# Kernel optimization log

Measured on AMD Instinct MI355X. Metric: run time of the kernel, lower is better.

## Reference

```python
import jax, jax.numpy as jnp
import numpy as np


def setup_inputs() -> dict:
    key = jax.random.key(0)
    # [3, B, H, N, d] stacked q, k, v
    qkv = jax.random.normal(key, (3, 4, 8, 4096, 32), dtype=jnp.float32)
    return {"qkv": qkv}


def reference(qkv):
    q, k, v = qkv[0], qkv[1], qkv[2]  # each [B, H, N, d]
    # kv_mod = box(k,k)^T @ v  -> [B,H,d,d,d] (avoids materializing [B,H,N,d^2])
    kv2 = jnp.einsum('bhnd,bhne,bhnf->bhdef', k, k, v)
    # k^T @ v -> [B,H,d,d]
    kv1 = jnp.einsum('bhnd,bhnf->bhdf', k, v)
    v_sum = jnp.sum(v, axis=-2, keepdims=True)  # [B,H,1,d]
    k_sum = jnp.sum(k, axis=-2)                 # [B,H,d]
    # y = 0.5 * box(q,q) @ kv_mod + q @ (k^T v) + sum(v)
    y = (0.5 * jnp.einsum('bhnd,bhne,bhdef->bhnf', q, q, kv2)
         + jnp.einsum('bhnd,bhdf->bhnf', q, kv1)
         + v_sum)
    # y_norm: box(q,q) . box(k_sum,k_sum) == (q . k_sum)^2
    qk = jnp.einsum('bhnd,bhd->bhn', q, k_sum)  # [B,H,N]
    y_norm = 0.5 * qk * qk + qk + 1.0
    return y / y_norm[..., None]
```

## Files before the change

kernel.cpp:

```cpp
#include <hip/hip_runtime.h>

#define NTOK 4096
#define DIM 32
#define NBH 32

#define BHF1 18496
#define SLOT1 591872
#define SUMOFF1 18432
#define KCH1 16
#define TSF 260
#define TSH 264

#define KCH 18
#define PK_U32 (NBH * KCH * 1024)
#define PK_HALF (PK_U32 / 2)
#define P2TOK 128

#define NPAIR2 528
#define NROWS 560
#define BHF (NROWS * 32 + 64)
#define SLOT (NBH * BHF)
#define TILE 64
#define LSTR 36
#define P1T 320

typedef __attribute__((ext_vector_type(8))) short bf16x8;
typedef __attribute__((ext_vector_type(8))) _Float16 f16x8;
typedef __attribute__((ext_vector_type(4))) float f32x4;
typedef __attribute__((ext_vector_type(4))) unsigned u32x4;

__device__ __forceinline__ int tri_start(int d) { return (d * (65 - d)) >> 1; }

__device__ __forceinline__ int tri_decode_d(int p) {
    int d = (int)((65.0f - sqrtf((float)(4225 - 8 * p))) * 0.5f);
    if (d < 0) d = 0;
    if (d > 31) d = 31;
    while (d < 31 && tri_start(d + 1) <= p) ++d;
    while (d > 0 && tri_start(d) > p) --d;
    return d;
}

__device__ __forceinline__ void row_operands(int row, int& ia, int& ib) {
    if (row < NPAIR2) {
        const int d = tri_decode_d(row);
        ia = d; ib = d + (row - tri_start(d));
    } else if (row < NROWS) {
        ia = row - NPAIR2; ib = 32;
    } else {
        ia = 34; ib = 34;
    }
}

__device__ __forceinline__ unsigned short f2bf(float x) {
    unsigned u = __builtin_bit_cast(unsigned, x);
    return (unsigned short)((u + 0x7FFFu + ((u >> 16) & 1u)) >> 16);
}
__device__ __forceinline__ float bf2f(unsigned short u) {
    return __builtin_bit_cast(float, (unsigned)u << 16);
}

__device__ __forceinline__ void split8(const float* p, f16x8& hi, f16x8& lo) {
#pragma unroll
    for (int j = 0; j < 8; ++j) {
        const _Float16 h = (_Float16)p[j];
        hi[j] = h;
        lo[j] = (_Float16)(p[j] - (float)h);
    }
}

#define MF(A, B, C) __builtin_amdgcn_mfma_f32_16x16x32_f16((A), (B), (C), 0, 0, 0)

__global__ __launch_bounds__(256) void phase1m_kernel(const float* __restrict__ qkv,
                                                      float* __restrict__ ws) {
    const int chunk = blockIdx.x;
    const int bh = blockIdx.y;
    const int t = threadIdx.x;
    const int w = t >> 6, l = t & 63, g = l >> 4, c16 = l & 15;

    __shared__ float skT[32 * TSF];
    __shared__ _Float16 svhiT[32 * TSH];
    __shared__ _Float16 svloT[32 * TSH];

    {
        const float4* kg4 = (const float4*)(qkv + (size_t)(NBH + bh) * (NTOK * DIM) + (size_t)chunk * 256 * DIM);
        const float4* vg4 = (const float4*)(qkv + (size_t)(2 * NBH + bh) * (NTOK * DIM) + (size_t)chunk * 256 * DIM);
#pragma unroll
        for (int j = 0; j < 8; ++j) {
            const int i = t + 256 * j;
            const int tok = i >> 3, dbase = (i & 7) << 2;
            const float4 kf = kg4[i];
            const float4 vf = vg4[i];
            const float ke[4] = {kf.x, kf.y, kf.z, kf.w};
            const float ve[4] = {vf.x, vf.y, vf.z, vf.w};
#pragma unroll
            for (int c = 0; c < 4; ++c) {
                skT[(dbase + c) * TSF + tok] = ke[c];
                const _Float16 h = (_Float16)ve[c];
                svhiT[(dbase + c) * TSH + tok] = h;
                svloT[(dbase + c) * TSH + tok] = (_Float16)(ve[c] - (float)h);
            }
        }
    }
    __syncthreads();

    f32x4 acc[4][2][2];
    f32x4 accS[2][2];
#pragma unroll
    for (int i = 0; i < 4; ++i)
#pragma unroll
        for (int m = 0; m < 2; ++m)
#pragma unroll
            for (int fh = 0; fh < 2; ++fh) acc[i][m][fh] = (f32x4){0.f, 0.f, 0.f, 0.f};
#pragma unroll
    for (int m = 0; m < 2; ++m)
#pragma unroll
        for (int fh = 0; fh < 2; ++fh) accS[m][fh] = (f32x4){0.f, 0.f, 0.f, 0.f};

    const f16x8 ones = {(_Float16)1.f, (_Float16)1.f, (_Float16)1.f, (_Float16)1.f,
                        (_Float16)1.f, (_Float16)1.f, (_Float16)1.f, (_Float16)1.f};

#pragma unroll 1
    for (int n0 = 0; n0 < 256; n0 += 32) {
        const int sl = n0 + 8 * g;
        float a0[8], a1[8];
        *(float4*)&a0[0] = *(const float4*)(skT + c16 * TSF + sl);
        *(float4*)&a0[4] = *(const float4*)(skT + c16 * TSF + sl + 4);
        *(float4*)&a1[0] = *(const float4*)(skT + (16 + c16) * TSF + sl);
        *(float4*)&a1[4] = *(const float4*)(skT + (16 + c16) * TSF + sl + 4);
        const f16x8 Bh0 = *(const f16x8*)(svhiT + c16 * TSH + sl);
        const f16x8 Bh1 = *(const f16x8*)(svhiT + (16 + c16) * TSH + sl);
        const f16x8 Bl0 = *(const f16x8*)(svloT + c16 * TSH + sl);
        const f16x8 Bl1 = *(const f16x8*)(svloT + (16 + c16) * TSH + sl);

#pragma unroll
        for (int i = 0; i < 4; ++i) {
            const int o = w + 4 * i;
            const int r0 = ((c16 + o) & 31) * TSF;
            const int r1 = ((16 + c16 + o) & 31) * TSF;
            float e0[8], e1[8], p0[8], p1[8];
            *(float4*)&e0[0] = *(const float4*)(skT + r0 + sl);
            *(float4*)&e0[4] = *(const float4*)(skT + r0 + sl + 4);
            *(float4*)&e1[0] = *(const float4*)(skT + r1 + sl);
            *(float4*)&e1[4] = *(const float4*)(skT + r1 + sl + 4);
#pragma unroll
            for (int j = 0; j < 8; ++j) { p0[j] = a0[j] * e0[j]; p1[j] = a1[j] * e1[j]; }
            f16x8 A0h, A0l, A1h, A1l;
            split8(p0, A0h, A0l);
            split8(p1, A1h, A1l);
            acc[i][0][0] = MF(A0h, Bh0, acc[i][0][0]);
            acc[i][0][0] = MF(A0l, Bh0, acc[i][0][0]);
            acc[i][0][0] = MF(A0h, Bl0, acc[i][0][0]);
            acc[i][0][1] = MF(A0h, Bh1, acc[i][0][1]);
            acc[i][0][1] = MF(A0l, Bh1, acc[i][0][1]);
            acc[i][0][1] = MF(A0h, Bl1, acc[i][0][1]);
            acc[i][1][0] = MF(A1h, Bh0, acc[i][1][0]);
            acc[i][1][0] = MF(A1l, Bh0, acc[i][1][0]);
            acc[i][1][0] = MF(A1h, Bl0, acc[i][1][0]);
            acc[i][1][1] = MF(A1h, Bh1, acc[i][1][1]);
            acc[i][1][1] = MF(A1l, Bh1, acc[i][1][1]);
            acc[i][1][1] = MF(A1h, Bl1, acc[i][1][1]);
        }

        if (w == 0) {
            float p[8];
#pragma unroll
            for (int j = 0; j < 8; ++j) p[j] = a0[j] * a1[j];
            f16x8 Ah, Al;
            split8(p, Ah, Al);
            accS[0][0] = MF(Ah, Bh0, accS[0][0]);
            accS[0][0] = MF(Al, Bh0, accS[0][0]);
            accS[0][0] = MF(Ah, Bl0, accS[0][0]);
            accS[0][1] = MF(Ah, Bh1, accS[0][1]);
            accS[0][1] = MF(Al, Bh1, accS[0][1]);
            accS[0][1] = MF(Ah, Bl1, accS[0][1]);
        } else if (w == 1) {
            f16x8 K0h, K0l, K1h, K1l;
            split8(a0, K0h, K0l);
            split8(a1, K1h, K1l);
            accS[0][0] = MF(K0h, Bh0, accS[0][0]);
            accS[0][0] = MF(K0l, Bh0, accS[0][0]);
            accS[0][0] = MF(K0h, Bl0, accS[0][0]);
            accS[0][1] = MF(K0h, Bh1, accS[0][1]);
            accS[0][1] = MF(K0l, Bh1, accS[0][1]);
            accS[0][1] = MF(K0h, Bl1, accS[0][1]);
            accS[1][0] = MF(K1h, Bh0, accS[1][0]);
            accS[1][0] = MF(K1l, Bh0, accS[1][0]);
            accS[1][0] = MF(K1h, Bl0, accS[1][0]);
            accS[1][1] = MF(K1h, Bh1, accS[1][1]);
            accS[1][1] = MF(K1l, Bh1, accS[1][1]);
            accS[1][1] = MF(K1h, Bl1, accS[1][1]);
        } else if (w == 2) {
            f16x8 K0h, K0l, K1h, K1l;
            split8(a0, K0h, K0l);
            split8(a1, K1h, K1l);
            accS[0][0] = MF(ones, K0h, accS[0][0]);
            accS[0][0] = MF(ones, K0l, accS[0][0]);
            accS[1][0] = MF(ones, K1h, accS[1][0]);
            accS[1][0] = MF(ones, K1l, accS[1][0]);
        } else {
            accS[0][0] = MF(ones, Bh0, accS[0][0]);
            accS[0][0] = MF(ones, Bl0, accS[0][0]);
            accS[0][1] = MF(ones, Bh1, accS[0][1]);
            accS[0][1] = MF(ones, Bl1, accS[0][1]);
        }
    }

    float* pb = ws + (size_t)SLOT1 * (1 + chunk) + (size_t)bh * BHF1;
#pragma unroll
    for (int i = 0; i < 4; ++i) {
        const int o = w + 4 * i;
#pragma unroll
        for (int m = 0; m < 2; ++m)
#pragma unroll
            for (int fh = 0; fh < 2; ++fh)
#pragma unroll
                for (int r = 0; r < 4; ++r) {
                    const int R = o * 32 + 16 * m + 4 * g + r;
                    pb[(size_t)R * 32 + fh * 16 + c16] = acc[i][m][fh][r];
                }
    }
    if (w == 0) {
#pragma unroll
        for (int fh = 0; fh < 2; ++fh)
#pragma unroll
            for (int r = 0; r < 4; ++r) {
                const int R = 512 + 4 * g + r;
                pb[(size_t)R * 32 + fh * 16 + c16] = accS[0][fh][r];
                pb[(size_t)(R + 16) * 32 + fh * 16 + c16] = accS[0][fh][r];
            }
    } else if (w == 1) {
#pragma unroll
        for (int m = 0; m < 2; ++m)
#pragma unroll
            for (int fh = 0; fh < 2; ++fh)
#pragma unroll
                for (int r = 0; r < 4; ++r) {
                    const int R = 544 + 16 * m + 4 * g + r;
                    pb[(size_t)R * 32 + fh * 16 + c16] = accS[m][fh][r];
                }
    } else if (w == 2) {
        if (g == 0) {
            pb[SUMOFF1 + c16] = accS[0][0][0];
            pb[SUMOFF1 + 16 + c16] = accS[1][0][0];
        }
    } else {
        if (g == 0) {
            pb[SUMOFF1 + 32 + c16] = accS[0][0][0];
            pb[SUMOFF1 + 48 + c16] = accS[0][1][0];
        }
    }
}

__global__ __launch_bounds__(256) void reduceprep_kernel(const float* __restrict__ ws,
                                                         float* __restrict__ wsw,
                                                         unsigned* __restrict__ bpk) {
    const int tid = blockIdx.x * 256 + threadIdx.x;
    if (tid < PK_HALF) {
        const int r = tid & 3;
        const int l = (tid >> 2) & 63;
        const int fh = (tid >> 8) & 1;
        const int kcbh = tid >> 9;
        const int kc = kcbh % KCH;
        const int bh = kcbh / KCH;
        const int f = fh * 16 + (l & 15);
        const int k0 = kc * 32 + ((l >> 4) << 3) + 2 * r;
        const float scale = (kc == 0 || kc == 16) ? 0.5f : 1.0f;
        float va = 0.f, vb = 0.f;
        const float* src = ws + (size_t)bh * BHF1 + (size_t)k0 * 32 + f;
#pragma unroll
        for (int c = 1; c <= KCH1; ++c) {
            va += src[(size_t)SLOT1 * c];
            vb += src[(size_t)SLOT1 * c + 32];
        }
        va *= scale; vb *= scale;
        const _Float16 ha = (_Float16)va, hb = (_Float16)vb;
        const _Float16 la = (_Float16)(va - (float)ha), lb = (_Float16)(vb - (float)hb);
        const int widx = ((bh * KCH + kc) * 2 + fh) * 512 + l * 4 + r;
        bpk[widx] = (unsigned)__builtin_bit_cast(unsigned short, ha) |
                    ((unsigned)__builtin_bit_cast(unsigned short, hb) << 16);
        bpk[widx + 256] = (unsigned)__builtin_bit_cast(unsigned short, la) |
                          ((unsigned)__builtin_bit_cast(unsigned short, lb) << 16);
    } else {
        const int tid2 = tid - PK_HALF;
        if (tid2 < NBH * 64) {
            const int bh = tid2 >> 6;
            const int j = tid2 & 63;
            float s = 0.f;
            const float* src = ws + (size_t)bh * BHF1 + SUMOFF1 + j;
#pragma unroll
            for (int c = 1; c <= KCH1; ++c) s += src[(size_t)SLOT1 * c];
            wsw[(size_t)bh * BHF1 + SUMOFF1 + j] = s;
        }
    }
}

#define EMIT_PHI() do { \
    unsigned hh[16]; \
    _Pragma("unroll") \
    for (int kp = 0; kp < 16; ++kp) { \
        const _Float16 h0 = (_Float16)phi[2 * kp]; \
        const _Float16 h1 = (_Float16)phi[2 * kp + 1]; \
        hh[kp] = (unsigned)__builtin_bit_cast(unsigned short, h0) | \
                 ((unsigned)__builtin_bit_cast(unsigned short, h1) << 16); \
    } \
    _Pragma("unroll") \
    for (int c4 = 0; c4 < 4; ++c4) { \
        u32x4 vh = {hh[4*c4], hh[4*c4+1], hh[4*c4+2], hh[4*c4+3]}; \
        *(u32x4*)&sph[t * 20 + c4 * 4] = vh; \
    } \
} while (0)

#define MFMA_CHUNK(KC) do { \
    const unsigned* bc = bbase + (size_t)(KC) * 1024; \
    const f16x8 Bh0 = __builtin_bit_cast(f16x8, *(const u32x4*)(bc + 0   + l * 4)); \
    const f16x8 Bl0 = __builtin_bit_cast(f16x8, *(const u32x4*)(bc + 256 + l * 4)); \
    const f16x8 Bh1 = __builtin_bit_cast(f16x8, *(const u32x4*)(bc + 512 + l * 4)); \
    const f16x8 Bl1 = __builtin_bit_cast(f16x8, *(const u32x4*)(bc + 768 + l * 4)); \
    _Pragma("unroll") \
    for (int T = 0; T < 4; ++T) { \
        const int ro = (wbase + T * 16 + arow) * 20 + acol; \
        const f16x8 Ah = __builtin_bit_cast(f16x8, *(const u32x4*)&sph[ro]); \
        acc[T][0] = MF(Ah, Bh0, acc[T][0]); \
        acc[T][0] = MF(Ah, Bl0, acc[T][0]); \
        acc[T][1] = MF(Ah, Bh1, acc[T][1]); \
        acc[T][1] = MF(Ah, Bl1, acc[T][1]); \
    } \
} while (0)

__global__ __launch_bounds__(P2TOK) void phase2m_kernel(const float* __restrict__ qkv,
                                                        const float* __restrict__ ws,
                                                        const unsigned* __restrict__ bpk,
                                                        float* __restrict__ out) {
    const int bh = blockIdx.y;
    const int tok0 = blockIdx.x * P2TOK;
    const int t = threadIdx.x;
    const int l = t & 63;
    const int wbase = (t >> 6) << 6;
    const int arow = l & 15;
    const int acol = (l >> 4) << 2;

    __shared__ unsigned sph[P2TOK * 20];
    __shared__ float sinv[P2TOK];

    float q[32];
    {
        const float4* q4 = (const float4*)(qkv + ((size_t)bh * NTOK + tok0 + t) * DIM);
#pragma unroll
        for (int i = 0; i < 8; ++i) {
            const float4 v = q4[i];
            q[4 * i + 0] = v.x; q[4 * i + 1] = v.y; q[4 * i + 2] = v.z; q[4 * i + 3] = v.w;
        }
    }
    {
        const float* ks = ws + (size_t)bh * BHF1 + SUMOFF1;
        float qk = 0.f;
#pragma unroll
        for (int d = 0; d < 32; ++d) qk += q[d] * ks[d];
        sinv[t] = 1.0f / (0.5f * qk * qk + qk + 1.0f);
    }

    f32x4 acc[4][2];
#pragma unroll
    for (int T = 0; T < 4; ++T)
#pragma unroll
        for (int fh = 0; fh < 2; ++fh) acc[T][fh] = (f32x4){0.f, 0.f, 0.f, 0.f};

    const unsigned* bbase = bpk + (size_t)bh * (KCH * 1024);

    {
        float qr[32];
#pragma unroll
        for (int j2 = 0; j2 < 32; ++j2) qr[j2] = q[j2];
#pragma unroll 1
        for (int kc = 0; kc < 17; ++kc) {
            float phi[32];
#pragma unroll
            for (int j2 = 0; j2 < 32; ++j2) phi[j2] = q[j2] * qr[j2];
            EMIT_PHI();
            MFMA_CHUNK(kc);
            const float tmp = qr[0];
#pragma unroll
            for (int j2 = 0; j2 < 31; ++j2) qr[j2] = qr[j2 + 1];
            qr[31] = tmp;
        }
    }
    {
        float phi[32];
#pragma unroll
        for (int j2 = 0; j2 < 32; ++j2) phi[j2] = q[j2];
        EMIT_PHI();
        MFMA_CHUNK(17);
    }

    const float* vs = ws + (size_t)bh * BHF1 + SUMOFF1 + 32;
    const float vs0 = vs[l & 15];
    const float vs1 = vs[16 + (l & 15)];
#pragma unroll
    for (int T = 0; T < 4; ++T) {
#pragma unroll
        for (int r = 0; r < 4; ++r) {
            const int row = wbase + T * 16 + ((l >> 4) << 2) + r;
            const float iv = sinv[row];
            float* op = out + ((size_t)bh * NTOK + tok0 + row) * DIM + (l & 15);
            op[0]  = (acc[T][0][r] + vs0) * iv;
            op[16] = (acc[T][1][r] + vs1) * iv;
        }
    }
}

__global__ __launch_bounds__(P1T) void phase1_kernel(const float* __restrict__ qkv,
                                                     float* __restrict__ ws, int direct) {
    const int chunk = blockIdx.x;
    const int bh = blockIdx.y;
    const int CHt = NTOK / gridDim.x;
    const int t = threadIdx.x;
    const float* kptr = qkv + (size_t)(NBH + bh) * (NTOK * DIM);
    const float* vptr = qkv + (size_t)(2 * NBH + bh) * (NTOK * DIM);
    float* base = ws + (direct ? (size_t)0 : (size_t)SLOT * (1 + chunk)) + (size_t)bh * BHF;

    __shared__ __align__(16) float sk[TILE][LSTR];
    __shared__ __align__(16) float sv[TILE][LSTR];

    int ia0, ib0, ia1, ib1;
    row_operands(t, ia0, ib0);
    row_operands(t + P1T, ia1, ib1);
    const float* a0 = &sk[0][ia0];
    const float* b0 = &sk[0][ib0];
    const float* a1 = &sk[0][ia1];
    const float* b1 = &sk[0][ib1];
    const float* sums = (t >= 288) ? &sv[0][t - 288] : ((t >= 256) ? &sk[0][t - 256] : &sk[0][0]);

    float acc0[32], acc1[32];
#pragma unroll
    for (int f = 0; f < 32; ++f) { acc0[f] = 0.f; acc1[f] = 0.f; }
    float accs = 0.f;

    if (t < 64) sk[t][32] = 1.0f;
    else if (t < 128) sk[t - 64][34] = 0.0f;

    const int n0 = chunk * CHt;
    for (int nt = 0; nt < CHt; nt += TILE) {
        __syncthreads();
        if (t < 256) {
            const float4* kg4 = (const float4*)(kptr + (size_t)(n0 + nt) * DIM);
            const float4* vg4 = (const float4*)(vptr + (size_t)(n0 + nt) * DIM);
            const int i0 = t, i1 = t + 256;
            *(float4*)&sk[i0 >> 3][(i0 & 7) << 2] = kg4[i0];
            *(float4*)&sk[i1 >> 3][(i1 & 7) << 2] = kg4[i1];
            *(float4*)&sv[i0 >> 3][(i0 & 7) << 2] = vg4[i0];
            *(float4*)&sv[i1 >> 3][(i1 & 7) << 2] = vg4[i1];
        }
        __syncthreads();
#pragma unroll 2
        for (int nn = 0; nn < TILE; ++nn) {
            const float s0 = a0[nn * LSTR] * b0[nn * LSTR];
            const float s1 = a1[nn * LSTR] * b1[nn * LSTR];
            const float* vrow = vptr + (size_t)(n0 + nt + nn) * DIM;
            float4 w[8];
#pragma unroll
            for (int j = 0; j < 8; ++j) w[j] = ((const float4*)vrow)[j];
#pragma unroll
            for (int j = 0; j < 8; ++j) {
                acc0[4 * j + 0] += s0 * w[j].x; acc0[4 * j + 1] += s0 * w[j].y;
                acc0[4 * j + 2] += s0 * w[j].z; acc0[4 * j + 3] += s0 * w[j].w;
                acc1[4 * j + 0] += s1 * w[j].x; acc1[4 * j + 1] += s1 * w[j].y;
                acc1[4 * j + 2] += s1 * w[j].z; acc1[4 * j + 3] += s1 * w[j].w;
            }
            if (t >= 256) accs += sums[nn * LSTR];
        }
    }

    {
        float* dst = base + (size_t)t * 32;
#pragma unroll
        for (int j = 0; j < 8; ++j) {
            float4 v; v.x = acc0[4 * j]; v.y = acc0[4 * j + 1];
            v.z = acc0[4 * j + 2]; v.w = acc0[4 * j + 3];
            ((float4*)dst)[j] = v;
        }
    }
    if (t < 240) {
        float* dst = base + (size_t)(t + P1T) * 32;
#pragma unroll
        for (int j = 0; j < 8; ++j) {
            float4 v; v.x = acc1[4 * j]; v.y = acc1[4 * j + 1];
            v.z = acc1[4 * j + 2]; v.w = acc1[4 * j + 3];
            ((float4*)dst)[j] = v;
        }
    }
    if (t >= 256) base[NROWS * 32 + (t - 256)] = accs;
}

__global__ __launch_bounds__(256) void phase2_kernel(const float* __restrict__ qkv,
                                                     const float* __restrict__ ws,
                                                     float* __restrict__ out) {
    const int bh = blockIdx.y;
    const int f0 = blockIdx.z << 4;
    const int t = threadIdx.x;
    const int tok0 = blockIdx.x * 256;
    const float* qptr = qkv + (size_t)bh * (NTOK * DIM) + (size_t)tok0 * DIM;
    const float* base = ws + (size_t)bh * BHF;
    const float* ksum = base + NROWS * 32;
    const float* vsum = ksum + 32;

    __shared__ float qT[32][256];
    {
        const float4* q4 = (const float4*)qptr + (size_t)t * 8;
#pragma unroll
        for (int i = 0; i < 8; ++i) {
            const float4 v = q4[i];
            qT[4 * i + 0][t] = v.x; qT[4 * i + 1][t] = v.y;
            qT[4 * i + 2][t] = v.z; qT[4 * i + 3][t] = v.w;
        }
    }
    __syncthreads();

    float y[16];
#pragma unroll
    for (int j = 0; j < 4; ++j) {
        const float4 v = *(const float4*)(vsum + f0 + 4 * j);
        y[4 * j + 0] = v.x; y[4 * j + 1] = v.y; y[4 * j + 2] = v.z; y[4 * j + 3] = v.w;
    }
    float qk = 0.f;
    const float* rowp = base + f0;
#pragma unroll 1
    for (int d = 0; d < 32; ++d) {
        const float qd = qT[d][t];
        qk += qd * ksum[d];
        {
            const float s = 0.5f * qd * qd;
            const float4* r = (const float4*)rowp;
#pragma unroll
            for (int j = 0; j < 4; ++j) {
                const float4 w = r[j];
                y[4 * j + 0] += s * w.x; y[4 * j + 1] += s * w.y;
                y[4 * j + 2] += s * w.z; y[4 * j + 3] += s * w.w;
            }
            rowp += 32;
        }
#pragma unroll 4
        for (int e = d + 1; e < 32; ++e) {
            const float s = qd * qT[e][t];
            const float4* r = (const float4*)rowp;
#pragma unroll
            for (int j = 0; j < 4; ++j) {
                const float4 w = r[j];
                y[4 * j + 0] += s * w.x; y[4 * j + 1] += s * w.y;
                y[4 * j + 2] += s * w.z; y[4 * j + 3] += s * w.w;
            }
            rowp += 32;
        }
    }
#pragma unroll 4
    for (int d = 0; d < 32; ++d) {
        const float qd = qT[d][t];
        const float4* r = (const float4*)rowp;
#pragma unroll
        for (int j = 0; j < 4; ++j) {
            const float4 w = r[j];
            y[4 * j + 0] += qd * w.x; y[4 * j + 1] += qd * w.y;
            y[4 * j + 2] += qd * w.z; y[4 * j + 3] += qd * w.w;
        }
        rowp += 32;
    }
    const float inv = 1.0f / (0.5f * qk * qk + qk + 1.0f);
    float4* o4 = (float4*)(out + (size_t)bh * (NTOK * DIM) + (size_t)(tok0 + t) * DIM + f0);
#pragma unroll
    for (int j = 0; j < 4; ++j) {
        float4 v;
        v.x = y[4 * j + 0] * inv; v.y = y[4 * j + 1] * inv;
        v.z = y[4 * j + 2] * inv; v.w = y[4 * j + 3] * inv;
        o4[j] = v;
    }
}

extern "C" void kernel_launch(void* const* d_in, const int* in_sizes, int n_in,
                              void* d_out, int out_size, void* d_ws, size_t ws_size,
                              hipStream_t stream) {
    const float* qkv = (const float*)d_in[0];
    float* out = (float*)d_out;
    float* ws = (float*)d_ws;

    const size_t need = ((size_t)(1 + KCH1) * SLOT1 + PK_U32) * 4;
    if (ws_size >= need) {
        unsigned* bpk = (unsigned*)(ws + (size_t)(1 + KCH1) * SLOT1);
        phase1m_kernel<<<dim3(KCH1, NBH), dim3(256), 0, stream>>>(qkv, ws);
        reduceprep_kernel<<<dim3((PK_HALF + NBH * 64) / 256), dim3(256), 0, stream>>>(ws, ws, bpk);
        phase2m_kernel<<<dim3(NTOK / P2TOK, NBH), dim3(P2TOK), 0, stream>>>(qkv, ws, bpk, out);
    } else {
        phase1_kernel<<<dim3(1, NBH), dim3(P1T), 0, stream>>>(qkv, ws, 1);
        phase2_kernel<<<dim3(NTOK / 256, NBH, 2), dim3(256), 0, stream>>>(qkv, ws, out);
    }
}
```

Before: 62.84 us.

## Halve phase1 LDS staging, vectorize transposed stores, shrink phase2 blocks to one wave

Phase1 now stages K/V in two 128-token halves instead of one 256-token tile. Each thread loads four tokens for one feature quad and writes transposed rows with vector stores, which halves LDS use and replaces scalar transposed writes. Phase2 drops to 64 tokens per block (a single wave) and unrolls the feature-chunk loop by four, removing per-iteration register rotation. The changes add extra barriers in phase1 and launch twice as many smaller phase2 blocks.

```diff
diff --git a/kernel.cpp b/kernel.cpp
--- a/kernel.cpp
+++ b/kernel.cpp
@@ -8,13 +8,13 @@
 #define SLOT1 591872
 #define SUMOFF1 18432
 #define KCH1 16
-#define TSF 260
-#define TSH 264
+#define TSF2 132
+#define TSH2 136
 
 #define KCH 18
 #define PK_U32 (NBH * KCH * 1024)
 #define PK_HALF (PK_U32 / 2)
-#define P2TOK 128
+#define P2TOK 64
 
 #define NPAIR2 528
 #define NROWS 560
@@ -26,6 +26,7 @@
 
 typedef __attribute__((ext_vector_type(8))) short bf16x8;
 typedef __attribute__((ext_vector_type(8))) _Float16 f16x8;
+typedef __attribute__((ext_vector_type(4))) _Float16 f16x4;
 typedef __attribute__((ext_vector_type(4))) float f32x4;
 typedef __attribute__((ext_vector_type(4))) unsigned u32x4;
 
@@ -51,14 +52,6 @@
     }
 }
 
-__device__ __forceinline__ unsigned short f2bf(float x) {
-    unsigned u = __builtin_bit_cast(unsigned, x);
-    return (unsigned short)((u + 0x7FFFu + ((u >> 16) & 1u)) >> 16);
-}
-__device__ __forceinline__ float bf2f(unsigned short u) {
-    return __builtin_bit_cast(float, (unsigned)u << 16);
-}
-
 __device__ __forceinline__ void split8(const float* p, f16x8& hi, f16x8& lo) {
 #pragma unroll
     for (int j = 0; j < 8; ++j) {
@@ -77,31 +70,12 @@
     const int t = threadIdx.x;
     const int w = t >> 6, l = t & 63, g = l >> 4, c16 = l & 15;
 
-    __shared__ float skT[32 * TSF];
-    __shared__ _Float16 svhiT[32 * TSH];
-    __shared__ _Float16 svloT[32 * TSH];
-
-    {
-        const float4* kg4 = (const float4*)(qkv + (size_t)(NBH + bh) * (NTOK * DIM) + (size_t)chunk * 256 * DIM);
-        const float4* vg4 = (const float4*)(qkv + (size_t)(2 * NBH + bh) * (NTOK * DIM) + (size_t)chunk * 256 * DIM);
-#pragma unroll
-        for (int j = 0; j < 8; ++j) {
-            const int i = t + 256 * j;
-            const int tok = i >> 3, dbase = (i & 7) << 2;
-            const float4 kf = kg4[i];
-            const float4 vf = vg4[i];
-            const float ke[4] = {kf.x, kf.y, kf.z, kf.w};
-            const float ve[4] = {vf.x, vf.y, vf.z, vf.w};
-#pragma unroll
-            for (int c = 0; c < 4; ++c) {
-                skT[(dbase + c) * TSF + tok] = ke[c];
-                const _Float16 h = (_Float16)ve[c];
-                svhiT[(dbase + c) * TSH + tok] = h;
-                svloT[(dbase + c) * TSH + tok] = (_Float16)(ve[c] - (float)h);
-            }
-        }
-    }
-    __syncthreads();
+    __shared__ float skT[32 * TSF2];
+    __shared__ _Float16 svhiT[32 * TSH2];
+    __shared__ _Float16 svloT[32 * TSH2];
+
+    const float4* kg4 = (const float4*)(qkv + (size_t)(NBH + bh) * (NTOK * DIM)) + (size_t)chunk * 256 * 8;
+    const float4* vg4 = (const float4*)(qkv + (size_t)(2 * NBH + bh) * (NTOK * DIM)) + (size_t)chunk * 256 * 8;
 
     f32x4 acc[4][2][2];
     f32x4 accS[2][2];
@@ -119,89 +93,129 @@
     const f16x8 ones = {(_Float16)1.f, (_Float16)1.f, (_Float16)1.f, (_Float16)1.f,
                         (_Float16)1.f, (_Float16)1.f, (_Float16)1.f, (_Float16)1.f};
 
+    const int fq = t >> 5;
+    const int tq = t & 31;
+
 #pragma unroll 1
-    for (int n0 = 0; n0 < 256; n0 += 32) {
-        const int sl = n0 + 8 * g;
-        float a0[8], a1[8];
-        *(float4*)&a0[0] = *(const float4*)(skT + c16 * TSF + sl);
-        *(float4*)&a0[4] = *(const float4*)(skT + c16 * TSF + sl + 4);
-        *(float4*)&a1[0] = *(const float4*)(skT + (16 + c16) * TSF + sl);
-        *(float4*)&a1[4] = *(const float4*)(skT + (16 + c16) * TSF + sl + 4);
-        const f16x8 Bh0 = *(const f16x8*)(svhiT + c16 * TSH + sl);
-        const f16x8 Bh1 = *(const f16x8*)(svhiT + (16 + c16) * TSH + sl);
-        const f16x8 Bl0 = *(const f16x8*)(svloT + c16 * TSH + sl);
-        const f16x8 Bl1 = *(const f16x8*)(svloT + (16 + c16) * TSH + sl);
-
-#pragma unroll
-        for (int i = 0; i < 4; ++i) {
-            const int o = w + 4 * i;
-            const int r0 = ((c16 + o) & 31) * TSF;
-            const int r1 = ((16 + c16 + o) & 31) * TSF;
-            float e0[8], e1[8], p0[8], p1[8];
-            *(float4*)&e0[0] = *(const float4*)(skT + r0 + sl);
-            *(float4*)&e0[4] = *(const float4*)(skT + r0 + sl + 4);
-            *(float4*)&e1[0] = *(const float4*)(skT + r1 + sl);
-            *(float4*)&e1[4] = *(const float4*)(skT + r1 + sl + 4);
-#pragma unroll
-            for (int j = 0; j < 8; ++j) { p0[j] = a0[j] * e0[j]; p1[j] = a1[j] * e1[j]; }
-            f16x8 A0h, A0l, A1h, A1l;
-            split8(p0, A0h, A0l);
-            split8(p1, A1h, A1l);
-            acc[i][0][0] = MF(A0h, Bh0, acc[i][0][0]);
-            acc[i][0][0] = MF(A0l, Bh0, acc[i][0][0]);
-            acc[i][0][0] = MF(A0h, Bl0, acc[i][0][0]);
-            acc[i][0][1] = MF(A0h, Bh1, acc[i][0][1]);
-            acc[i][0][1] = MF(A0l, Bh1, acc[i][0][1]);
-            acc[i][0][1] = MF(A0h, Bl1, acc[i][0][1]);
-            acc[i][1][0] = MF(A1h, Bh0, acc[i][1][0]);
-            acc[i][1][0] = MF(A1l, Bh0, acc[i][1][0]);
-            acc[i][1][0] = MF(A1h, Bl0, acc[i][1][0]);
-            acc[i][1][1] = MF(A1h, Bh1, acc[i][1][1]);
-            acc[i][1][1] = MF(A1l, Bh1, acc[i][1][1]);
-            acc[i][1][1] = MF(A1h, Bl1, acc[i][1][1]);
-        }
-
-        if (w == 0) {
-            float p[8];
-#pragma unroll
-            for (int j = 0; j < 8; ++j) p[j] = a0[j] * a1[j];
-            f16x8 Ah, Al;
-            split8(p, Ah, Al);
-            accS[0][0] = MF(Ah, Bh0, accS[0][0]);
-            accS[0][0] = MF(Al, Bh0, accS[0][0]);
-            accS[0][0] = MF(Ah, Bl0, accS[0][0]);
-            accS[0][1] = MF(Ah, Bh1, accS[0][1]);
-            accS[0][1] = MF(Al, Bh1, accS[0][1]);
-            accS[0][1] = MF(Ah, Bl1, accS[0][1]);
-        } else if (w == 1) {
-            f16x8 K0h, K0l, K1h, K1l;
-            split8(a0, K0h, K0l);
-            split8(a1, K1h, K1l);
-            accS[0][0] = MF(K0h, Bh0, accS[0][0]);
-            accS[0][0] = MF(K0l, Bh0, accS[0][0]);
-            accS[0][0] = MF(K0h, Bl0, accS[0][0]);
-            accS[0][1] = MF(K0h, Bh1, accS[0][1]);
-            accS[0][1] = MF(K0l, Bh1, accS[0][1]);
-            accS[0][1] = MF(K0h, Bl1, accS[0][1]);
-            accS[1][0] = MF(K1h, Bh0, accS[1][0]);
-            accS[1][0] = MF(K1l, Bh0, accS[1][0]);
-            accS[1][0] = MF(K1h, Bl0, accS[1][0]);
-            accS[1][1] = MF(K1h, Bh1, accS[1][1]);
-            accS[1][1] = MF(K1l, Bh1, accS[1][1]);
-            accS[1][1] = MF(K1h, Bl1, accS[1][1]);
-        } else if (w == 2) {
-            f16x8 K0h, K0l, K1h, K1l;
-            split8(a0, K0h, K0l);
-            split8(a1, K1h, K1l);
-            accS[0][0] = MF(ones, K0h, accS[0][0]);
-            accS[0][0] = MF(ones, K0l, accS[0][0]);
-            accS[1][0] = MF(ones, K1h, accS[1][0]);
-            accS[1][0] = MF(ones, K1l, accS[1][0]);
-        } else {
-            accS[0][0] = MF(ones, Bh0, accS[0][0]);
-            accS[0][0] = MF(ones, Bl0, accS[0][0]);
-            accS[0][1] = MF(ones, Bh1, accS[0][1]);
-            accS[0][1] = MF(ones, Bl1, accS[0][1]);
+    for (int half = 0; half < 2; ++half) {
+        __syncthreads();
+        {
+            const int nb = half * 128;
+            float4 kf[4], vf[4];
+#pragma unroll
+            for (int c = 0; c < 4; ++c) {
+                kf[c] = kg4[(size_t)(nb + tq * 4 + c) * 8 + fq];
+                vf[c] = vg4[(size_t)(nb + tq * 4 + c) * 8 + fq];
+            }
+            const float kr[4][4] = {{kf[0].x, kf[1].x, kf[2].x, kf[3].x},
+                                    {kf[0].y, kf[1].y, kf[2].y, kf[3].y},
+                                    {kf[0].z, kf[1].z, kf[2].z, kf[3].z},
+                                    {kf[0].w, kf[1].w, kf[2].w, kf[3].w}};
+            const float vr[4][4] = {{vf[0].x, vf[1].x, vf[2].x, vf[3].x},
+                                    {vf[0].y, vf[1].y, vf[2].y, vf[3].y},
+                                    {vf[0].z, vf[1].z, vf[2].z, vf[3].z},
+                                    {vf[0].w, vf[1].w, vf[2].w, vf[3].w}};
+#pragma unroll
+            for (int r = 0; r < 4; ++r) {
+                *(float4*)(skT + (fq * 4 + r) * TSF2 + tq * 4) =
+                    (float4){kr[r][0], kr[r][1], kr[r][2], kr[r][3]};
+                f16x4 vh, vl;
+#pragma unroll
+                for (int c = 0; c < 4; ++c) {
+                    const _Float16 h = (_Float16)vr[r][c];
+                    vh[c] = h;
+                    vl[c] = (_Float16)(vr[r][c] - (float)h);
+                }
+                *(f16x4*)(svhiT + (fq * 4 + r) * TSH2 + tq * 4) = vh;
+                *(f16x4*)(svloT + (fq * 4 + r) * TSH2 + tq * 4) = vl;
+            }
+        }
+        __syncthreads();
+
+#pragma unroll 1
+        for (int it = 0; it < 4; ++it) {
+            const int sl = it * 32 + 8 * g;
+            float a0[8], a1[8];
+            *(float4*)&a0[0] = *(const float4*)(skT + c16 * TSF2 + sl);
+            *(float4*)&a0[4] = *(const float4*)(skT + c16 * TSF2 + sl + 4);
+            *(float4*)&a1[0] = *(const float4*)(skT + (16 + c16) * TSF2 + sl);
+            *(float4*)&a1[4] = *(const float4*)(skT + (16 + c16) * TSF2 + sl + 4);
+            const f16x8 Bh0 = *(const f16x8*)(svhiT + c16 * TSH2 + sl);
+            const f16x8 Bh1 = *(const f16x8*)(svhiT + (16 + c16) * TSH2 + sl);
+            const f16x8 Bl0 = *(const f16x8*)(svloT + c16 * TSH2 + sl);
+            const f16x8 Bl1 = *(const f16x8*)(svloT + (16 + c16) * TSH2 + sl);
+
+#pragma unroll
+            for (int i = 0; i < 4; ++i) {
+                const int o = w + 4 * i;
+                const int r0 = ((c16 + o) & 31) * TSF2;
+                const int r1 = ((16 + c16 + o) & 31) * TSF2;
+                float e0[8], e1[8], p0[8], p1[8];
+                *(float4*)&e0[0] = *(const float4*)(skT + r0 + sl);
+                *(float4*)&e0[4] = *(const float4*)(skT + r0 + sl + 4);
+                *(float4*)&e1[0] = *(const float4*)(skT + r1 + sl);
+                *(float4*)&e1[4] = *(const float4*)(skT + r1 + sl + 4);
+#pragma unroll
+                for (int j = 0; j < 8; ++j) { p0[j] = a0[j] * e0[j]; p1[j] = a1[j] * e1[j]; }
+                f16x8 A0h, A0l, A1h, A1l;
+                split8(p0, A0h, A0l);
+                split8(p1, A1h, A1l);
+                acc[i][0][0] = MF(A0h, Bh0, acc[i][0][0]);
+                acc[i][0][0] = MF(A0l, Bh0, acc[i][0][0]);
+                acc[i][0][0] = MF(A0h, Bl0, acc[i][0][0]);
+                acc[i][0][1] = MF(A0h, Bh1, acc[i][0][1]);
+                acc[i][0][1] = MF(A0l, Bh1, acc[i][0][1]);
+                acc[i][0][1] = MF(A0h, Bl1, acc[i][0][1]);
+                acc[i][1][0] = MF(A1h, Bh0, acc[i][1][0]);
+                acc[i][1][0] = MF(A1l, Bh0, acc[i][1][0]);
+                acc[i][1][0] = MF(A1h, Bl0, acc[i][1][0]);
+                acc[i][1][1] = MF(A1h, Bh1, acc[i][1][1]);
+                acc[i][1][1] = MF(A1l, Bh1, acc[i][1][1]);
+                acc[i][1][1] = MF(A1h, Bl1, acc[i][1][1]);
+            }
+
+            if (w == 0) {
+                float p[8];
+#pragma unroll
+                for (int j = 0; j < 8; ++j) p[j] = a0[j] * a1[j];
+                f16x8 Ah, Al;
+                split8(p, Ah, Al);
+                accS[0][0] = MF(Ah, Bh0, accS[0][0]);
+                accS[0][0] = MF(Al, Bh0, accS[0][0]);
+                accS[0][0] = MF(Ah, Bl0, accS[0][0]);
+                accS[0][1] = MF(Ah, Bh1, accS[0][1]);
+                accS[0][1] = MF(Al, Bh1, accS[0][1]);
+                accS[0][1] = MF(Ah, Bl1, accS[0][1]);
+            } else if (w == 1) {
+                f16x8 K0h, K0l, K1h, K1l;
+                split8(a0, K0h, K0l);
+                split8(a1, K1h, K1l);
+                accS[0][0] = MF(K0h, Bh0, accS[0][0]);
+                accS[0][0] = MF(K0l, Bh0, accS[0][0]);
+                accS[0][0] = MF(K0h, Bl0, accS[0][0]);
+                accS[0][1] = MF(K0h, Bh1, accS[0][1]);
+                accS[0][1] = MF(K0l, Bh1, accS[0][1]);
+                accS[0][1] = MF(K0h, Bl1, accS[0][1]);
+                accS[1][0] = MF(K1h, Bh0, accS[1][0]);
+                accS[1][0] = MF(K1l, Bh0, accS[1][0]);
+                accS[1][0] = MF(K1h, Bl0, accS[1][0]);
+                accS[1][1] = MF(K1h, Bh1, accS[1][1]);
+                accS[1][1] = MF(K1l, Bh1, accS[1][1]);
+                accS[1][1] = MF(K1h, Bl1, accS[1][1]);
+            } else if (w == 2) {
+                f16x8 K0h, K0l, K1h, K1l;
+                split8(a0, K0h, K0l);
+                split8(a1, K1h, K1l);
+                accS[0][0] = MF(ones, K0h, accS[0][0]);
+                accS[0][0] = MF(ones, K0l, accS[0][0]);
+                accS[1][0] = MF(ones, K1h, accS[1][0]);
+                accS[1][0] = MF(ones, K1l, accS[1][0]);
+            } else {
+                accS[0][0] = MF(ones, Bh0, accS[0][0]);
+                accS[0][0] = MF(ones, Bl0, accS[0][0]);
+                accS[0][1] = MF(ones, Bh1, accS[0][1]);
+                accS[0][1] = MF(ones, Bl1, accS[0][1]);
+            }
         }
     }
 
@@ -294,31 +308,31 @@
     }
 }
 
-#define EMIT_PHI() do { \
+#define EMIT_MFMA(PHIEXPR, KCEXPR) do { \
     unsigned hh[16]; \
     _Pragma("unroll") \
     for (int kp = 0; kp < 16; ++kp) { \
-        const _Float16 h0 = (_Float16)phi[2 * kp]; \
-        const _Float16 h1 = (_Float16)phi[2 * kp + 1]; \
+        const int j0 = 2 * kp, j1 = 2 * kp + 1; \
+        const float p0 = (PHIEXPR(j0)); \
+        const float p1 = (PHIEXPR(j1)); \
+        const _Float16 h0 = (_Float16)p0; \
+        const _Float16 h1 = (_Float16)p1; \
         hh[kp] = (unsigned)__builtin_bit_cast(unsigned short, h0) | \
                  ((unsigned)__builtin_bit_cast(unsigned short, h1) << 16); \
     } \
     _Pragma("unroll") \
     for (int c4 = 0; c4 < 4; ++c4) { \
-        u32x4 vh = {hh[4*c4], hh[4*c4+1], hh[4*c4+2], hh[4*c4+3]}; \
+        u32x4 vh = {hh[4 * c4], hh[4 * c4 + 1], hh[4 * c4 + 2], hh[4 * c4 + 3]}; \
         *(u32x4*)&sph[t * 20 + c4 * 4] = vh; \
     } \
-} while (0)
-
-#define MFMA_CHUNK(KC) do { \
-    const unsigned* bc = bbase + (size_t)(KC) * 1024; \
-    const f16x8 Bh0 = __builtin_bit_cast(f16x8, *(const u32x4*)(bc + 0   + l * 4)); \
-    const f16x8 Bl0 = __builtin_bit_cast(f16x8, *(const u32x4*)(bc + 256 + l * 4)); \
-    const f16x8 Bh1 = __builtin_bit_cast(f16x8, *(const u32x4*)(bc + 512 + l * 4)); \
-    const f16x8 Bl1 = __builtin_bit_cast(f16x8, *(const u32x4*)(bc + 768 + l * 4)); \
+    const unsigned* bc = bbase + (size_t)(KCEXPR) * 1024; \
+    const f16x8 Bh0 = __builtin_bit_cast(f16x8, *(const u32x4*)(bc + 0   + t * 4)); \
+    const f16x8 Bl0 = __builtin_bit_cast(f16x8, *(const u32x4*)(bc + 256 + t * 4)); \
+    const f16x8 Bh1 = __builtin_bit_cast(f16x8, *(const u32x4*)(bc + 512 + t * 4)); \
+    const f16x8 Bl1 = __builtin_bit_cast(f16x8, *(const u32x4*)(bc + 768 + t * 4)); \
     _Pragma("unroll") \
     for (int T = 0; T < 4; ++T) { \
-        const int ro = (wbase + T * 16 + arow) * 20 + acol; \
+        const int ro = (T * 16 + arow) * 20 + acol; \
         const f16x8 Ah = __builtin_bit_cast(f16x8, *(const u32x4*)&sph[ro]); \
         acc[T][0] = MF(Ah, Bh0, acc[T][0]); \
         acc[T][0] = MF(Ah, Bl0, acc[T][0]); \
@@ -334,10 +348,8 @@
     const int bh = blockIdx.y;
     const int tok0 = blockIdx.x * P2TOK;
     const int t = threadIdx.x;
-    const int l = t & 63;
-    const int wbase = (t >> 6) << 6;
-    const int arow = l & 15;
-    const int acol = (l >> 4) << 2;
+    const int arow = t & 15;
+    const int acol = (t >> 4) << 2;
 
     __shared__ unsigned sph[P2TOK * 20];
     __shared__ float sinv[P2TOK];
@@ -367,41 +379,50 @@
 
     const unsigned* bbase = bpk + (size_t)bh * (KCH * 1024);
 
+    float qr[32];
+#pragma unroll
+    for (int j = 0; j < 32; ++j) qr[j] = q[j];
+
+#pragma unroll 1
+    for (int kc4 = 0; kc4 < 16; kc4 += 4) {
+#define PHI_S0(J) (q[(J)] * qr[(J)])
+#define PHI_S1(J) (q[(J)] * qr[((J) + 1) & 31])
+#define PHI_S2(J) (q[(J)] * qr[((J) + 2) & 31])
+#define PHI_S3(J) (q[(J)] * qr[((J) + 3) & 31])
+        EMIT_MFMA(PHI_S0, kc4 + 0);
+        EMIT_MFMA(PHI_S1, kc4 + 1);
+        EMIT_MFMA(PHI_S2, kc4 + 2);
+        EMIT_MFMA(PHI_S3, kc4 + 3);
+#undef PHI_S0
+#undef PHI_S1
+#undef PHI_S2
+#undef PHI_S3
+        const float t0 = qr[0], t1 = qr[1], t2 = qr[2], t3 = qr[3];
+#pragma unroll
+        for (int j = 0; j < 28; ++j) qr[j] = qr[j + 4];
+        qr[28] = t0; qr[29] = t1; qr[30] = t2; qr[31] = t3;
+    }
     {
-        float qr[32];
-#pragma unroll
-        for (int j2 = 0; j2 < 32; ++j2) qr[j2] = q[j2];
-#pragma unroll 1
-        for (int kc = 0; kc < 17; ++kc) {
-            float phi[32];
-#pragma unroll
-            for (int j2 = 0; j2 < 32; ++j2) phi[j2] = q[j2] * qr[j2];
-            EMIT_PHI();
-            MFMA_CHUNK(kc);
-            const float tmp = qr[0];
-#pragma unroll
-            for (int j2 = 0; j2 < 31; ++j2) qr[j2] = qr[j2 + 1];
-            qr[31] = tmp;
-        }
+#define PHI_16(J) (q[(J)] * qr[(J)])
+        EMIT_MFMA(PHI_16, 16);
+#undef PHI_16
     }
     {
-        float phi[32];
-#pragma unroll
-        for (int j2 = 0; j2 < 32; ++j2) phi[j2] = q[j2];
-        EMIT_PHI();
-        MFMA_CHUNK(17);
+#define PHI_Q(J) (q[(J)])
+        EMIT_MFMA(PHI_Q, 17);
+#undef PHI_Q
     }
 
     const float* vs = ws + (size_t)bh * BHF1 + SUMOFF1 + 32;
-    const float vs0 = vs[l & 15];
-    const float vs1 = vs[16 + (l & 15)];
+    const float vs0 = vs[t & 15];
+    const float vs1 = vs[16 + (t & 15)];
 #pragma unroll
     for (int T = 0; T < 4; ++T) {
 #pragma unroll
         for (int r = 0; r < 4; ++r) {
-            const int row = wbase + T * 16 + ((l >> 4) << 2) + r;
+            const int row = T * 16 + ((t >> 4) << 2) + r;
             const float iv = sinv[row];
-            float* op = out + ((size_t)bh * NTOK + tok0 + row) * DIM + (l & 15);
+            float* op = out + ((size_t)bh * NTOK + tok0 + row) * DIM + (t & 15);
             op[0]  = (acc[T][0][r] + vs0) * iv;
             op[16] = (acc[T][1][r] + vs1) * iv;
         }
```

Result: faster. 61.36 us (-2.3%).
